# Kernel optimization log

Measured on AMD Instinct MI355X. Metric: run time of the kernel, lower is better.

## Reference

```python
import jax, jax.numpy as jnp
import numpy as np

NUM_HEADS = 12
HEAD_DIM = 64
HIDDEN = 768
SLOT_DIM = 30
BS = 8
FULL = SLOT_DIM * BS  # 240
SLOT_LEN = 32
LEN0 = 512   # slot-broadcast cache length
LEN1 = 128   # per-sample cache length


def tf_slot(x, slot_dim):
    # (slot_dim*bs, H, L, h) -> (bs, H, slot_dim*L, h)
    full, nh, L, h = x.shape
    bs = full // slot_dim
    x = x.reshape(slot_dim, bs, nh, L, h).transpose(1, 2, 0, 3, 4)
    return x.reshape(bs, nh, slot_dim * L, h)


def back_slot(x, slot_dim):
    # (bs, H, slot_dim*L, h) -> (slot_dim*bs, H, L, h)
    bs, nh, total, h = x.shape
    L = total // slot_dim
    x = x.reshape(bs, nh, slot_dim, L, h).transpose(2, 0, 1, 3, 4)
    return x.reshape(slot_dim * bs, nh, L, h)


def setup_inputs() -> dict:
    key = jax.random.key(0)
    ks = jax.random.split(key, 12)
    s = 0.02
    return {
        "hidden_states": jax.random.normal(ks[0], (FULL, SLOT_LEN, HIDDEN), jnp.float32),
        "attention_mask": jnp.zeros((FULL, 1, 1, LEN0 + LEN1 + SLOT_LEN), jnp.float32),
        "cache0_key": jax.random.normal(ks[1], (BS, NUM_HEADS, LEN0, HEAD_DIM), jnp.float32),
        "cache0_value": jax.random.normal(ks[2], (BS, NUM_HEADS, LEN0, HEAD_DIM), jnp.float32),
        "cache1_key": jax.random.normal(ks[3], (FULL, NUM_HEADS, LEN1, HEAD_DIM), jnp.float32),
        "cache1_value": jax.random.normal(ks[4], (FULL, NUM_HEADS, LEN1, HEAD_DIM), jnp.float32),
        "Wq": jax.random.normal(ks[5], (HIDDEN, HIDDEN), jnp.float32) * s,
        "bq": jax.random.normal(ks[6], (HIDDEN,), jnp.float32) * s,
        "Wk": jax.random.normal(ks[7], (HIDDEN, HIDDEN), jnp.float32) * s,
        "bk": jax.random.normal(ks[8], (HIDDEN,), jnp.float32) * s,
        "Wv": jax.random.normal(ks[9], (HIDDEN, HIDDEN), jnp.float32) * s,
        "bv": jax.random.normal(ks[10], (HIDDEN,), jnp.float32) * s,
        "slot_dim": SLOT_DIM,
    }


def reference(hidden_states, attention_mask, cache0_key, cache0_value,
              cache1_key, cache1_value, Wq, bq, Wk, bk, Wv, bv, slot_dim):
    B, L, hid = hidden_states.shape

    def split_heads(x):  # (B, L, hid) -> (B, H, L, h)
        return x.reshape(B, L, NUM_HEADS, HEAD_DIM).transpose(0, 2, 1, 3)

    q = split_heads(hidden_states @ Wq + bq)
    k = split_heads(hidden_states @ Wk + bk)
    v = split_heads(hidden_states @ Wv + bv)

    # self-attention scores (B, H, L, L)
    self_scores = jnp.einsum('bhqd,bhkd->bhqk', q, k)

    # cache0: slot-broadcast path (cache batch = bs, queries batch = slot_dim*bs)
    q_tf = tf_slot(q, slot_dim)  # (bs, H, slot_dim*L, h)
    s0 = back_slot(jnp.einsum('bhqd,bhkd->bhqk', q_tf, cache0_key), slot_dim)  # (B,H,L,LEN0)
    # cache1: direct path (matching batch)
    s1 = jnp.einsum('bhqd,bhkd->bhqk', q, cache1_key)  # (B,H,L,LEN1)

    scores = jnp.concatenate([s0, s1, self_scores], axis=-1)
    scores = scores / jnp.sqrt(jnp.float32(HEAD_DIM)) + attention_mask
    probs = jax.nn.softmax(scores, axis=-1)  # single softmax over all KV sources

    len0 = cache0_key.shape[2]
    len1 = cache1_key.shape[2]
    # self context
    ctx = jnp.einsum('bhqk,bhkd->bhqd', probs[..., -L:], v)
    # cache0 context via slot transform
    p0 = tf_slot(probs[..., :len0], slot_dim)  # (bs, H, slot_dim*L, LEN0)
    ctx = ctx + back_slot(jnp.einsum('bhqk,bhkd->bhqd', p0, cache0_value), slot_dim)
    # cache1 context direct
    ctx = ctx + jnp.einsum('bhqk,bhkd->bhqd', probs[..., len0:len0 + len1], cache1_value)

    # (B, H, L, h) -> (B, L, hid)
    return ctx.transpose(0, 2, 1, 3).reshape(B, L, hid)
```

## Files before the change

### kernel.cpp

```cpp
#include <hip/hip_runtime.h>
#include <math.h>

#define NUM_HEADS 12
#define HEAD_DIM  64
#define HIDDEN    768
#define BS        8
#define FULL      240
#define SLOT_LEN  32
#define LEN0      512
#define LEN1      128
#define KTOT      672
#define M_TOK     (FULL * SLOT_LEN)

typedef float f32x4 __attribute__((ext_vector_type(4)));
typedef short s16x8 __attribute__((ext_vector_type(8)));
typedef short s16x4 __attribute__((ext_vector_type(4)));

__device__ __forceinline__ short f2bf(float x) {
    unsigned u = __float_as_uint(x);
    unsigned r = (u + 0x7fffu + ((u >> 16) & 1u)) >> 16;
    return (short)r;
}

__device__ __forceinline__ void gll16(const short* g, short* l) {
    __builtin_amdgcn_global_load_lds(
        (const __attribute__((address_space(1))) unsigned int*)g,
        (__attribute__((address_space(3))) unsigned int*)l, 16, 0, 0);
}

__global__ __launch_bounds__(256) void cast_hs(const float* __restrict__ in,
                                               short* __restrict__ out, int n4) {
    int i = blockIdx.x * 256 + threadIdx.x;
    if (i < n4) {
        float4 v = ((const float4*)in)[i];
        s16x4 o = {f2bf(v.x), f2bf(v.y), f2bf(v.z), f2bf(v.w)};
        ((s16x4*)out)[i] = o;
    }
}

__global__ __launch_bounds__(256) void prep_c0(const float* __restrict__ k0,
                                               const float* __restrict__ v0,
                                               short* __restrict__ k0c,
                                               short* __restrict__ v0t) {
    __shared__ float tile[32][65];
    const size_t base = (size_t)blockIdx.x * 2048;
    const int t = threadIdx.x;
    if (blockIdx.y == 0) {
        const int row = t >> 3, c8 = t & 7;
        const float* src = &k0[base + row * 64 + c8 * 8];
        float4 a = *(const float4*)src;
        float4 b = *(const float4*)(src + 4);
        s16x8 o = {f2bf(a.x), f2bf(a.y), f2bf(a.z), f2bf(a.w),
                   f2bf(b.x), f2bf(b.y), f2bf(b.z), f2bf(b.w)};
        *(s16x8*)&k0c[base + row * 64 + (size_t)((c8 ^ (row & 7)) * 8)] = o;
    } else {
#pragma unroll
        for (int i = 0; i < 2; ++i) {
            int f = t + i * 256;
            int kr = f >> 4, d4 = (f & 15) * 4;
            float4 v = *(const float4*)&v0[base + kr * 64 + d4];
            tile[kr][d4 + 0] = v.x; tile[kr][d4 + 1] = v.y;
            tile[kr][d4 + 2] = v.z; tile[kr][d4 + 3] = v.w;
        }
        __syncthreads();
#pragma unroll
        for (int i = 0; i < 2; ++i) {
            int g = t + i * 256;
            int d = g >> 3, kr4 = (g & 7) * 4;
            s16x4 o = {f2bf(tile[kr4 + 0][d]), f2bf(tile[kr4 + 1][d]),
                       f2bf(tile[kr4 + 2][d]), f2bf(tile[kr4 + 3][d])};
            int grp = (kr4 >> 3) ^ ((d >> 1) & 3);
            *(s16x4*)&v0t[base + d * 32 + grp * 8 + (kr4 & 7)] = o;
        }
    }
}

__global__ __launch_bounds__(256) void cast_w_t(const float* __restrict__ Wq,
                                                const float* __restrict__ Wk,
                                                const float* __restrict__ Wv,
                                                short* __restrict__ WtAll) {
    const float* W = (blockIdx.z == 0) ? Wq : (blockIdx.z == 1) ? Wk : Wv;
    short* Wt = WtAll + (size_t)blockIdx.z * HIDDEN * HIDDEN;
    __shared__ __align__(16) float tile[32][33];
    const int kb0 = blockIdx.y * 32, nb0 = blockIdx.x * 32;
    const int r = threadIdx.x >> 3, c4 = (threadIdx.x & 7) * 4;
    float4 v = *(const float4*)&W[(size_t)(kb0 + r) * HIDDEN + nb0 + c4];
    tile[r][c4 + 0] = v.x; tile[r][c4 + 1] = v.y;
    tile[r][c4 + 2] = v.z; tile[r][c4 + 3] = v.w;
    __syncthreads();
    s16x4 o = {f2bf(tile[c4 + 0][r]), f2bf(tile[c4 + 1][r]),
               f2bf(tile[c4 + 2][r]), f2bf(tile[c4 + 3][r])};
    *(s16x4*)&Wt[(size_t)(nb0 + r) * HIDDEN + kb0 + c4] = o;
}

__global__ __launch_bounds__(256) void qkv_mfma(
    const short* __restrict__ hsb, const short* __restrict__ WtAll,
    const float* __restrict__ bq, const float* __restrict__ bk,
    const float* __restrict__ bv,
    short* __restrict__ qo, short* __restrict__ ko, short* __restrict__ vo)
{
    const int z = blockIdx.z;
    const short* Wt = WtAll + (size_t)z * HIDDEN * HIDDEN;
    const float* bias = (z == 0) ? bq : (z == 1) ? bk : bv;
    short* outp = (z == 0) ? qo : (z == 1) ? ko : vo;

    __shared__ __align__(16) short smem[128 * 128];
    short* As = smem;
    short* Bs = smem + 128 * 64;

    const int t = threadIdx.x;
    const int lane = t & 63, w = t >> 6;
    const int l15 = lane & 15, quad = lane >> 4;
    const int mBase = blockIdx.y * 128, nBase = blockIdx.x * 128;
    const int mw = (w & 1) * 64, nw = (w >> 1) * 64;

    const int srow_in = lane >> 3;
    const int scol8 = (lane & 7) ^ srow_in;

    f32x4 acc[4][4];
    const f32x4 z4 = {0.f, 0.f, 0.f, 0.f};
#pragma unroll
    for (int i = 0; i < 4; ++i)
#pragma unroll
        for (int j = 0; j < 4; ++j) acc[i][j] = z4;

    for (int kb = 0; kb < HIDDEN; kb += 64) {
        __syncthreads();
#pragma unroll
        for (int j = 0; j < 4; ++j) {
            int row = w * 32 + j * 8 + srow_in;
            gll16(&hsb[(size_t)(mBase + row) * HIDDEN + kb + scol8 * 8],
                  &As[(w * 32 + j * 8) * 64]);
            gll16(&Wt[(size_t)(nBase + row) * HIDDEN + kb + scol8 * 8],
                  &Bs[(w * 32 + j * 8) * 64]);
        }
        __syncthreads();
#pragma unroll
        for (int kc = 0; kc < 2; ++kc) {
            s16x8 a[4], b[4];
#pragma unroll
            for (int mt = 0; mt < 4; ++mt) {
                int row = mw + mt * 16 + l15;
                int c8 = (kc * 4 + quad) ^ (row & 7);
                a[mt] = *(const s16x8*)&As[row * 64 + c8 * 8];
            }
#pragma unroll
            for (int nt = 0; nt < 4; ++nt) {
                int row = nw + nt * 16 + l15;
                int c8 = (kc * 4 + quad) ^ (row & 7);
                b[nt] = *(const s16x8*)&Bs[row * 64 + c8 * 8];
            }
#pragma unroll
            for (int mt = 0; mt < 4; ++mt)
#pragma unroll
                for (int nt = 0; nt < 4; ++nt)
                    acc[mt][nt] = __builtin_amdgcn_mfma_f32_16x16x32_bf16(
                        a[mt], b[nt], acc[mt][nt], 0, 0, 0);
        }
    }

    __syncthreads();
#pragma unroll
    for (int nt = 0; nt < 4; ++nt) {
        float bvv = bias[nBase + nw + nt * 16 + l15];
        int col = nw + nt * 16 + l15;
#pragma unroll
        for (int mt = 0; mt < 4; ++mt)
#pragma unroll
            for (int r = 0; r < 4; ++r) {
                int row = mw + mt * 16 + quad * 4 + r;
                smem[row * 128 + col] = f2bf(acc[mt][nt][r] + bvv);
            }
    }
    __syncthreads();
#pragma unroll
    for (int i = 0; i < 8; ++i) {
        int f = t + i * 256;
        int row = f >> 4, c8 = (f & 15) * 8;
        uint4 val = *(const uint4*)&smem[row * 128 + c8];
        int m = mBase + row, n = nBase + c8;
        size_t dst = (((size_t)(m >> 5) * NUM_HEADS + (n >> 6)) * SLOT_LEN + (m & 31)) * 64 + (n & 63);
        *(uint4*)&outp[dst] = val;
    }
}

__global__ __launch_bounds__(256) void attn_mfma(
    const short* __restrict__ qb, const short* __restrict__ kbuf,
    const short* __restrict__ vbuf,
    const short* __restrict__ k0c, const short* __restrict__ v0t,
    const float* __restrict__ c1k, const float* __restrict__ c1v,
    const float* __restrict__ mask, float* __restrict__ out)
{
    __shared__ __align__(16) short sm_s[20480];

    const int t = threadIdx.x, lane = t & 63, w = t >> 6;
    const int task = blockIdx.x;
    const int B = task / 12, h = task % 12;
    const int l15 = lane & 15, quad = lane >> 4;

    const short* qp  = qb  + (size_t)(B * NUM_HEADS + h) * SLOT_LEN * 64;
    const short* ksp = kbuf + (size_t)(B * NUM_HEADS + h) * SLOT_LEN * 64;
    const short* vsp = vbuf + (size_t)(B * NUM_HEADS + h) * SLOT_LEN * 64;
    const short* k0p = k0c + (size_t)((B & 7) * NUM_HEADS + h) * LEN0 * 64;
    const short* v0p = v0t + (size_t)((B & 7) * NUM_HEADS + h) * LEN0 * 64;
    const float* k1p = c1k + (size_t)(B * NUM_HEADS + h) * LEN1 * 64;
    const float* v1p = c1v + (size_t)(B * NUM_HEADS + h) * LEN1 * 64;
    const float* mp  = mask + (size_t)B * KTOT;

    short (*K)[64] = (short(*)[64])(sm_s + w * 5120);
    short (*V)[32] = (short(*)[32])(sm_s + w * 5120 + 2048);
    short (*P)[32] = (short(*)[32])(sm_s + w * 5120 + 4096);
    short* Kf = sm_s + w * 5120;
    short* Vf = sm_s + w * 5120 + 2048;

    const int skey = lane >> 4;
    const int sc4 = (lane & 15) << 2;

    const float LOG2E = 1.4426950408889634f;
    const float SCL   = 0.125f * 1.4426950408889634f;

    s16x8 qf[2][2];
#pragma unroll
    for (int qh = 0; qh < 2; ++qh)
#pragma unroll
        for (int kc = 0; kc < 2; ++kc)
            qf[qh][kc] = *(const s16x8*)&qp[(qh * 16 + l15) * 64 + kc * 32 + quad * 8];

    const f32x4 z4 = {0.f, 0.f, 0.f, 0.f};
    f32x4 o[2][4];
    float lpart[2][4];
#pragma unroll
    for (int qh = 0; qh < 2; ++qh) {
#pragma unroll
        for (int dq = 0; dq < 4; ++dq) o[qh][dq] = z4;
#pragma unroll
        for (int r = 0; r < 4; ++r) lpart[qh][r] = 0.f;
    }

    auto qk_exp = [&](float mv0, float mv1) {
        f32x4 s[2][2];
#pragma unroll
        for (int qh = 0; qh < 2; ++qh)
#pragma unroll
            for (int kh = 0; kh < 2; ++kh) s[qh][kh] = z4;
#pragma unroll
        for (int kh = 0; kh < 2; ++kh) {
            int rowk = kh * 16 + l15;
            s16x8 kf0 = *(const s16x8*)&K[rowk][(quad ^ (rowk & 7)) * 8];
            s16x8 kf1 = *(const s16x8*)&K[rowk][((4 + quad) ^ (rowk & 7)) * 8];
#pragma unroll
            for (int qh = 0; qh < 2; ++qh) {
                s[qh][kh] = __builtin_amdgcn_mfma_f32_16x16x32_bf16(qf[qh][0], kf0, s[qh][kh], 0, 0, 0);
                s[qh][kh] = __builtin_amdgcn_mfma_f32_16x16x32_bf16(qf[qh][1], kf1, s[qh][kh], 0, 0, 0);
            }
        }
#pragma unroll
        for (int qh = 0; qh < 2; ++qh)
#pragma unroll
            for (int kh = 0; kh < 2; ++kh) {
                float mv = kh ? mv1 : mv0;
#pragma unroll
                for (int r = 0; r < 4; ++r) {
                    float p = exp2f(fmaf(s[qh][kh][r], SCL, mv));
                    lpart[qh][r] += p;
                    int prow = qh * 16 + quad * 4 + r;
                    int pswz = ((kh * 2 + (l15 >> 3)) ^ ((prow >> 1) & 3)) * 8 + (l15 & 7);
                    P[prow][pswz] = f2bf(p);
                }
            }
    };
    auto pv = [&]() {
#pragma unroll
        for (int qh = 0; qh < 2; ++qh) {
            int prow2 = qh * 16 + l15;
            int pg = (quad ^ ((l15 >> 1) & 3)) * 8;
            s16x4 plo = *(const s16x4*)&P[prow2][pg];
            s16x4 phi = *(const s16x4*)&P[prow2][pg + 4];
            s16x8 pf = __builtin_shufflevector(plo, phi, 0, 1, 2, 3, 4, 5, 6, 7);
#pragma unroll
            for (int dq = 0; dq < 4; ++dq) {
                int vrow = dq * 16 + l15;
                s16x8 vf = *(const s16x8*)&V[vrow][(quad ^ ((l15 >> 1) & 3)) * 8];
                o[qh][dq] = __builtin_amdgcn_mfma_f32_16x16x32_bf16(pf, vf, o[qh][dq], 0, 0, 0);
            }
        }
    };

    if (w == 3) {
#pragma unroll
        for (int i = 0; i < 8; ++i) {
            int key = i * 4 + skey;
            *(s16x4*)&K[key][((l15 >> 1) ^ (key & 7)) * 8 + (l15 & 1) * 4] =
                *(const s16x4*)&ksp[key * 64 + sc4];
        }
        short vtmp[32];
#pragma unroll
        for (int key = 0; key < 32; ++key) vtmp[key] = vsp[key * 64 + lane];
#pragma unroll
        for (int k4 = 0; k4 < 8; ++k4) {
            s16x4 vo4 = {vtmp[k4 * 4 + 0], vtmp[k4 * 4 + 1],
                         vtmp[k4 * 4 + 2], vtmp[k4 * 4 + 3]};
            int grp = (k4 >> 1) ^ ((lane >> 1) & 3);
            *(s16x4*)&V[lane][grp * 8 + (k4 & 1) * 4] = vo4;
        }
        float mv0 = mp[20 * 32 + l15] * LOG2E;
        float mv1 = mp[20 * 32 + 16 + l15] * LOG2E;
        qk_exp(mv0, mv1);
        pv();
    }

    {
        int c = 16 + w;
        const float* sk = k1p + (c - 16) * 2048;
        const float* sv = v1p + (c - 16) * 2048;
        float4 kr[4], vv[4];
#pragma unroll
        for (int i = 0; i < 4; ++i)
            kr[i] = *(const float4*)&sk[(i * 4 + skey) * 64 + sc4];
#pragma unroll
        for (int i = 0; i < 4; ++i)
            vv[i] = *(const float4*)&sv[(i * 4 + skey) * 64 + sc4];
#pragma unroll
        for (int i = 0; i < 4; ++i) {
            s16x4 kk = {f2bf(kr[i].x), f2bf(kr[i].y), f2bf(kr[i].z), f2bf(kr[i].w)};
            int row = i * 4 + skey;
            *(s16x4*)&K[row][((l15 >> 1) ^ (row & 7)) * 8 + (l15 & 1) * 4] = kk;
        }
#pragma unroll
        for (int i = 0; i < 4; ++i)
            kr[i] = *(const float4*)&sk[((i + 4) * 4 + skey) * 64 + sc4];
#pragma unroll
        for (int i = 0; i < 4; ++i) {
            s16x4 kk = {f2bf(kr[i].x), f2bf(kr[i].y), f2bf(kr[i].z), f2bf(kr[i].w)};
            int row = (i + 4) * 4 + skey;
            *(s16x4*)&K[row][((l15 >> 1) ^ (row & 7)) * 8 + (l15 & 1) * 4] = kk;
        }
        float mv0 = mp[c * 32 + l15] * LOG2E;
        float mv1 = mp[c * 32 + 16 + l15] * LOG2E;
        qk_exp(mv0, mv1);
#pragma unroll
        for (int i = 0; i < 4; ++i) {
            int key = i * 4 + skey;
            int kg = key >> 3, ks = key & 7;
#pragma unroll
            for (int j = 0; j < 4; ++j) {
                int rowv = sc4 + j;
                float fv = (j == 0) ? vv[i].x : (j == 1) ? vv[i].y : (j == 2) ? vv[i].z : vv[i].w;
                V[rowv][(kg ^ ((rowv >> 1) & 3)) * 8 + ks] = f2bf(fv);
            }
        }
#pragma unroll
        for (int i = 0; i < 4; ++i)
            vv[i] = *(const float4*)&sv[((i + 4) * 4 + skey) * 64 + sc4];
#pragma unroll
        for (int i = 0; i < 4; ++i) {
            int key = (i + 4) * 4 + skey;
            int kg = key >> 3, ks = key & 7;
#pragma unroll
            for (int j = 0; j < 4; ++j) {
                int rowv = sc4 + j;
                float fv = (j == 0) ? vv[i].x : (j == 1) ? vv[i].y : (j == 2) ? vv[i].z : vv[i].w;
                V[rowv][(kg ^ ((rowv >> 1) & 3)) * 8 + ks] = f2bf(fv);
            }
        }
        pv();
    }

    {
        s16x8 kpre[4], vpre[4];
        const int cbase = w * 4;
        auto issue_bf = [&](int c) {
            const short* kcb = k0p + c * 2048;
            const short* vcb = v0p + c * 2048;
#pragma unroll
            for (int i = 0; i < 4; ++i) {
                kpre[i] = *(const s16x8*)&kcb[(i * 64 + lane) * 8];
                vpre[i] = *(const s16x8*)&vcb[(i * 64 + lane) * 8];
            }
        };
        issue_bf(cbase);
#pragma unroll
        for (int j = 0; j < 4; ++j) {
            int c = cbase + j;
#pragma unroll
            for (int i = 0; i < 4; ++i)
                *(s16x8*)&Kf[(i * 64 + lane) * 8] = kpre[i];
#pragma unroll
            for (int i = 0; i < 4; ++i)
                *(s16x8*)&Vf[(i * 64 + lane) * 8] = vpre[i];
            if (j + 1 < 4) issue_bf(c + 1);
            float mv0 = mp[c * 32 + l15] * LOG2E;
            float mv1 = mp[c * 32 + 16 + l15] * LOG2E;
            qk_exp(mv0, mv1);
            pv();
        }
    }

    float lred[2][4];
#pragma unroll
    for (int qh = 0; qh < 2; ++qh)
#pragma unroll
        for (int r = 0; r < 4; ++r) {
            float l = lpart[qh][r];
            l += __shfl_xor(l, 1);
            l += __shfl_xor(l, 2);
            l += __shfl_xor(l, 4);
            l += __shfl_xor(l, 8);
            lred[qh][r] = l;
        }

    __syncthreads();
    float* smf = (float*)sm_s;
#pragma unroll
    for (int qh = 0; qh < 2; ++qh)
#pragma unroll
        for (int dq = 0; dq < 4; ++dq)
#pragma unroll
            for (int r = 0; r < 4; ++r) {
                int row = qh * 16 + quad * 4 + r, col = dq * 16 + l15;
                smf[w * 2048 + row * 64 + col] = o[qh][dq][r];
            }
    if (l15 == 0) {
#pragma unroll
        for (int qh = 0; qh < 2; ++qh)
#pragma unroll
            for (int r = 0; r < 4; ++r)
                smf[8192 + w * 32 + qh * 16 + quad * 4 + r] = lred[qh][r];
    }
    __syncthreads();

    {
        int row = t >> 3, c8 = (t & 7) * 8;
        float lt = smf[8192 + row] + smf[8192 + 32 + row] +
                   smf[8192 + 64 + row] + smf[8192 + 96 + row];
        float inv = 1.f / lt;
        float4 o0, o1;
#pragma unroll
        for (int j = 0; j < 4; ++j) {
            int col = c8 + j;
            o0[j] = (smf[row * 64 + col] + smf[2048 + row * 64 + col] +
                     smf[4096 + row * 64 + col] + smf[6144 + row * 64 + col]) * inv;
        }
#pragma unroll
        for (int j = 0; j < 4; ++j) {
            int col = c8 + 4 + j;
            o1[j] = (smf[row * 64 + col] + smf[2048 + row * 64 + col] +
                     smf[4096 + row * 64 + col] + smf[6144 + row * 64 + col]) * inv;
        }
        float* op = &out[((size_t)B * SLOT_LEN + row) * HIDDEN + h * 64 + c8];
        *(float4*)op = o0;
        *(float4*)(op + 4) = o1;
    }
}

extern "C" void kernel_launch(void* const* d_in, const int* in_sizes, int n_in,
                              void* d_out, int out_size, void* d_ws, size_t ws_size,
                              hipStream_t stream) {
    const float* hs   = (const float*)d_in[0];
    const float* mask = (const float*)d_in[1];
    const float* c0k  = (const float*)d_in[2];
    const float* c0v  = (const float*)d_in[3];
    const float* c1k  = (const float*)d_in[4];
    const float* c1v  = (const float*)d_in[5];
    const float* Wq   = (const float*)d_in[6];
    const float* bq   = (const float*)d_in[7];
    const float* Wk   = (const float*)d_in[8];
    const float* bk   = (const float*)d_in[9];
    const float* Wv   = (const float*)d_in[10];
    const float* bv   = (const float*)d_in[11];
    float* out = (float*)d_out;

    short* hsb = (short*)d_ws;
    short* WtA = hsb + (size_t)M_TOK * HIDDEN;
    short* qb  = WtA + (size_t)3 * HIDDEN * HIDDEN;
    short* kbw = qb + (size_t)M_TOK * HIDDEN;
    short* vbw = kbw + (size_t)M_TOK * HIDDEN;
    short* k0c = (short*)d_ws;
    short* v0t = k0c + (size_t)BS * NUM_HEADS * LEN0 * HEAD_DIM;

    cast_hs<<<(M_TOK * HIDDEN / 4 + 255) / 256, 256, 0, stream>>>(hs, hsb, M_TOK * HIDDEN / 4);
    cast_w_t<<<dim3(24, 24, 3), 256, 0, stream>>>(Wq, Wk, Wv, WtA);
    qkv_mfma<<<dim3(HIDDEN / 128, M_TOK / 128, 3), 256, 0, stream>>>(
        hsb, WtA, bq, bk, bv, qb, kbw, vbw);
    prep_c0<<<dim3(BS * NUM_HEADS * (LEN0 / 32), 2), 256, 0, stream>>>(c0k, c0v, k0c, v0t);
    attn_mfma<<<FULL * NUM_HEADS, 256, 0, stream>>>(qb, kbw, vbw, k0c, v0t, c1k, c1v, mask, out);
}
```

Before: 369.3 us.

## Load attention K/V fragments straight into registers with MFMA-ready layouts

Cache0 V and the self-attention V are now written in an MFMA-fragment-ordered layout by the prep and QKV kernels, and K fragments are read directly from global memory. The attention kernel can therefore feed MFMAs from registers instead of staging K/V through LDS. Fragment loads are software-pipelined one chunk ahead. Only the cache1 path still goes through LDS, which shrinks the shared-memory footprint and may raise occupancy, at the cost of more register pressure and less coalesced global reads for K.

After: 359.8 us. 2.6% less time.

```diff
diff --git a/kernel.cpp b/kernel.cpp
--- a/kernel.cpp
+++ b/kernel.cpp
@@ -38,41 +38,31 @@
     }
 }
 
-__global__ __launch_bounds__(256) void prep_c0(const float* __restrict__ k0,
-                                               const float* __restrict__ v0,
-                                               short* __restrict__ k0c,
-                                               short* __restrict__ v0t) {
+__global__ __launch_bounds__(256) void prep_v0(const float* __restrict__ v0,
+                                               short* __restrict__ v0f) {
     __shared__ float tile[32][65];
     const size_t base = (size_t)blockIdx.x * 2048;
     const int t = threadIdx.x;
-    if (blockIdx.y == 0) {
-        const int row = t >> 3, c8 = t & 7;
-        const float* src = &k0[base + row * 64 + c8 * 8];
-        float4 a = *(const float4*)src;
-        float4 b = *(const float4*)(src + 4);
-        s16x8 o = {f2bf(a.x), f2bf(a.y), f2bf(a.z), f2bf(a.w),
-                   f2bf(b.x), f2bf(b.y), f2bf(b.z), f2bf(b.w)};
-        *(s16x8*)&k0c[base + row * 64 + (size_t)((c8 ^ (row & 7)) * 8)] = o;
-    } else {
-#pragma unroll
-        for (int i = 0; i < 2; ++i) {
-            int f = t + i * 256;
-            int kr = f >> 4, d4 = (f & 15) * 4;
-            float4 v = *(const float4*)&v0[base + kr * 64 + d4];
-            tile[kr][d4 + 0] = v.x; tile[kr][d4 + 1] = v.y;
-            tile[kr][d4 + 2] = v.z; tile[kr][d4 + 3] = v.w;
-        }
-        __syncthreads();
-#pragma unroll
-        for (int i = 0; i < 2; ++i) {
-            int g = t + i * 256;
-            int d = g >> 3, kr4 = (g & 7) * 4;
-            s16x4 o = {f2bf(tile[kr4 + 0][d]), f2bf(tile[kr4 + 1][d]),
-                       f2bf(tile[kr4 + 2][d]), f2bf(tile[kr4 + 3][d])};
-            int grp = (kr4 >> 3) ^ ((d >> 1) & 3);
-            *(s16x4*)&v0t[base + d * 32 + grp * 8 + (kr4 & 7)] = o;
-        }
-    }
+#pragma unroll
+    for (int i = 0; i < 2; ++i) {
+        int f = t + i * 256;
+        int kr = f >> 4, d4 = (f & 15) * 4;
+        float4 v = *(const float4*)&v0[base + kr * 64 + d4];
+        tile[kr][d4 + 0] = v.x; tile[kr][d4 + 1] = v.y;
+        tile[kr][d4 + 2] = v.z; tile[kr][d4 + 3] = v.w;
+    }
+    __syncthreads();
+    const int dq = t >> 6, lane = t & 63;
+    const int quad = lane >> 4, l15 = lane & 15;
+    s16x8 o = {f2bf(tile[quad * 8 + 0][dq * 16 + l15]),
+               f2bf(tile[quad * 8 + 1][dq * 16 + l15]),
+               f2bf(tile[quad * 8 + 2][dq * 16 + l15]),
+               f2bf(tile[quad * 8 + 3][dq * 16 + l15]),
+               f2bf(tile[quad * 8 + 4][dq * 16 + l15]),
+               f2bf(tile[quad * 8 + 5][dq * 16 + l15]),
+               f2bf(tile[quad * 8 + 6][dq * 16 + l15]),
+               f2bf(tile[quad * 8 + 7][dq * 16 + l15])};
+    *(s16x8*)&v0f[base + (size_t)t * 8] = o;
 }
 
 __global__ __launch_bounds__(256) void cast_w_t(const float* __restrict__ Wq,
@@ -104,7 +94,7 @@
     const float* bias = (z == 0) ? bq : (z == 1) ? bk : bv;
     short* outp = (z == 0) ? qo : (z == 1) ? ko : vo;
 
-    __shared__ __align__(16) short smem[128 * 128];
+    __shared__ __align__(16) short smem[128 * 144];
     short* As = smem;
     short* Bs = smem + 128 * 64;
 
@@ -169,49 +159,63 @@
 #pragma unroll
             for (int r = 0; r < 4; ++r) {
                 int row = mw + mt * 16 + quad * 4 + r;
-                smem[row * 128 + col] = f2bf(acc[mt][nt][r] + bvv);
-            }
-    }
-    __syncthreads();
-#pragma unroll
-    for (int i = 0; i < 8; ++i) {
-        int f = t + i * 256;
-        int row = f >> 4, c8 = (f & 15) * 8;
-        uint4 val = *(const uint4*)&smem[row * 128 + c8];
-        int m = mBase + row, n = nBase + c8;
-        size_t dst = (((size_t)(m >> 5) * NUM_HEADS + (n >> 6)) * SLOT_LEN + (m & 31)) * 64 + (n & 63);
-        *(uint4*)&outp[dst] = val;
+                short v = f2bf(acc[mt][nt][r] + bvv);
+                if (z == 2) smem[col * 144 + row] = v;
+                else        smem[row * 128 + col] = v;
+            }
+    }
+    __syncthreads();
+    if (z == 2) {
+#pragma unroll
+        for (int i = 0; i < 8; ++i) {
+            int f = t + i * 256;
+            int d = f >> 4, kb8 = (f & 15) * 8;
+            uint4 val = *(const uint4*)&smem[d * 144 + kb8];
+            int m0 = mBase + kb8, n = nBase + d;
+            int B = m0 >> 5, key0 = m0 & 31, hh = n >> 6, dd = n & 63;
+            size_t dst = ((size_t)(B * NUM_HEADS + hh) * 2048) +
+                         (size_t)((dd >> 4) * 512 + (key0 >> 3) * 128 + (dd & 15) * 8);
+            *(uint4*)&outp[dst] = val;
+        }
+    } else {
+#pragma unroll
+        for (int i = 0; i < 8; ++i) {
+            int f = t + i * 256;
+            int row = f >> 4, c8 = (f & 15) * 8;
+            uint4 val = *(const uint4*)&smem[row * 128 + c8];
+            int m = mBase + row, n = nBase + c8;
+            size_t dst = (((size_t)(m >> 5) * NUM_HEADS + (n >> 6)) * SLOT_LEN + (m & 31)) * 64 + (n & 63);
+            *(uint4*)&outp[dst] = val;
+        }
     }
 }
 
 __global__ __launch_bounds__(256) void attn_mfma(
     const short* __restrict__ qb, const short* __restrict__ kbuf,
     const short* __restrict__ vbuf,
-    const short* __restrict__ k0c, const short* __restrict__ v0t,
+    const short* __restrict__ k0c, const short* __restrict__ v0f,
     const float* __restrict__ c1k, const float* __restrict__ c1v,
     const float* __restrict__ mask, float* __restrict__ out)
 {
-    __shared__ __align__(16) short sm_s[20480];
+    __shared__ __align__(16) float smf[8448];
+    short* sm16 = (short*)smf;
 
     const int t = threadIdx.x, lane = t & 63, w = t >> 6;
     const int task = blockIdx.x;
     const int B = task / 12, h = task % 12;
     const int l15 = lane & 15, quad = lane >> 4;
 
-    const short* qp  = qb  + (size_t)(B * NUM_HEADS + h) * SLOT_LEN * 64;
-    const short* ksp = kbuf + (size_t)(B * NUM_HEADS + h) * SLOT_LEN * 64;
-    const short* vsp = vbuf + (size_t)(B * NUM_HEADS + h) * SLOT_LEN * 64;
-    const short* k0p = k0c + (size_t)((B & 7) * NUM_HEADS + h) * LEN0 * 64;
-    const short* v0p = v0t + (size_t)((B & 7) * NUM_HEADS + h) * LEN0 * 64;
-    const float* k1p = c1k + (size_t)(B * NUM_HEADS + h) * LEN1 * 64;
-    const float* v1p = c1v + (size_t)(B * NUM_HEADS + h) * LEN1 * 64;
-    const float* mp  = mask + (size_t)B * KTOT;
-
-    short (*K)[64] = (short(*)[64])(sm_s + w * 5120);
-    short (*V)[32] = (short(*)[32])(sm_s + w * 5120 + 2048);
-    short (*P)[32] = (short(*)[32])(sm_s + w * 5120 + 4096);
-    short* Kf = sm_s + w * 5120;
-    short* Vf = sm_s + w * 5120 + 2048;
+    const short* qp   = qb  + (size_t)(B * NUM_HEADS + h) * 2048;
+    const short* kspF = kbuf + (size_t)(B * NUM_HEADS + h) * 2048;
+    const short* vspF = vbuf + (size_t)(B * NUM_HEADS + h) * 2048;
+    const short* k0p  = k0c + (size_t)((B & 7) * NUM_HEADS + h) * LEN0 * 64;
+    const short* v0p  = v0f + (size_t)((B & 7) * NUM_HEADS + h) * LEN0 * 64;
+    const float* k1p  = c1k + (size_t)(B * NUM_HEADS + h) * LEN1 * 64;
+    const float* v1p  = c1v + (size_t)(B * NUM_HEADS + h) * LEN1 * 64;
+    const float* mp   = mask + (size_t)B * KTOT;
+
+    short (*V)[32] = (short(*)[32])(sm16 + w * 3072);
+    short (*P)[32] = (short(*)[32])(sm16 + w * 3072 + 2048);
 
     const int skey = lane >> 4;
     const int sc4 = (lane & 15) << 2;
@@ -237,23 +241,20 @@
         for (int r = 0; r < 4; ++r) lpart[qh][r] = 0.f;
     }
 
-    auto qk_exp = [&](float mv0, float mv1) {
-        f32x4 s[2][2];
+    auto qk_mm = [&](const s16x8* kf, f32x4 (*s)[2]) {
 #pragma unroll
         for (int qh = 0; qh < 2; ++qh)
 #pragma unroll
             for (int kh = 0; kh < 2; ++kh) s[qh][kh] = z4;
 #pragma unroll
-        for (int kh = 0; kh < 2; ++kh) {
-            int rowk = kh * 16 + l15;
-            s16x8 kf0 = *(const s16x8*)&K[rowk][(quad ^ (rowk & 7)) * 8];
-            s16x8 kf1 = *(const s16x8*)&K[rowk][((4 + quad) ^ (rowk & 7)) * 8];
+        for (int kh = 0; kh < 2; ++kh)
 #pragma unroll
             for (int qh = 0; qh < 2; ++qh) {
-                s[qh][kh] = __builtin_amdgcn_mfma_f32_16x16x32_bf16(qf[qh][0], kf0, s[qh][kh], 0, 0, 0);
-                s[qh][kh] = __builtin_amdgcn_mfma_f32_16x16x32_bf16(qf[qh][1], kf1, s[qh][kh], 0, 0, 0);
-            }
-        }
+                s[qh][kh] = __builtin_amdgcn_mfma_f32_16x16x32_bf16(qf[qh][0], kf[kh * 2 + 0], s[qh][kh], 0, 0, 0);
+                s[qh][kh] = __builtin_amdgcn_mfma_f32_16x16x32_bf16(qf[qh][1], kf[kh * 2 + 1], s[qh][kh], 0, 0, 0);
+            }
+    };
+    auto exp_p = [&](f32x4 (*s)[2], float mv0, float mv1) {
 #pragma unroll
         for (int qh = 0; qh < 2; ++qh)
 #pragma unroll
@@ -269,7 +270,7 @@
                 }
             }
     };
-    auto pv = [&]() {
+    auto pv_reg = [&](const s16x8* vf) {
 #pragma unroll
         for (int qh = 0; qh < 2; ++qh) {
             int prow2 = qh * 16 + l15;
@@ -278,6 +279,19 @@
             s16x4 phi = *(const s16x4*)&P[prow2][pg + 4];
             s16x8 pf = __builtin_shufflevector(plo, phi, 0, 1, 2, 3, 4, 5, 6, 7);
 #pragma unroll
+            for (int dq = 0; dq < 4; ++dq)
+                o[qh][dq] = __builtin_amdgcn_mfma_f32_16x16x32_bf16(pf, vf[dq], o[qh][dq], 0, 0, 0);
+        }
+    };
+    auto pv_lds = [&]() {
+#pragma unroll
+        for (int qh = 0; qh < 2; ++qh) {
+            int prow2 = qh * 16 + l15;
+            int pg = (quad ^ ((l15 >> 1) & 3)) * 8;
+            s16x4 plo = *(const s16x4*)&P[prow2][pg];
+            s16x4 phi = *(const s16x4*)&P[prow2][pg + 4];
+            s16x8 pf = __builtin_shufflevector(plo, phi, 0, 1, 2, 3, 4, 5, 6, 7);
+#pragma unroll
             for (int dq = 0; dq < 4; ++dq) {
                 int vrow = dq * 16 + l15;
                 s16x8 vf = *(const s16x8*)&V[vrow][(quad ^ ((l15 >> 1) & 3)) * 8];
@@ -286,114 +300,81 @@
         }
     };
 
-    if (w == 3) {
+    const int c0base = w * 4;
+    const int nfast = (w == 0) ? 5 : 4;
+
+    auto load_kf = [&](int i, s16x8* kf) {
+        const short* kb = (i < 4) ? (k0p + (size_t)(c0base + i) * 2048) : kspF;
+#pragma unroll
+        for (int f = 0; f < 4; ++f) {
+            int kh = f >> 1, kc = f & 1;
+            kf[f] = *(const s16x8*)&kb[(kh * 16 + l15) * 64 + kc * 32 + quad * 8];
+        }
+    };
+    auto load_vf = [&](int i, s16x8* vf) {
+        const short* vb = (i < 4) ? (v0p + (size_t)(c0base + i) * 2048) : vspF;
+#pragma unroll
+        for (int dq = 0; dq < 4; ++dq)
+            vf[dq] = *(const s16x8*)&vb[(dq * 64 + lane) * 8];
+    };
+    auto mchunk = [&](int i) { return (i < 4) ? (c0base + i) : 20; };
+
+    s16x8 kf[4], vf[4];
+    float mv0n, mv1n;
+    load_kf(0, kf);
+    load_vf(0, vf);
+    { int mc = mchunk(0); mv0n = mp[mc * 32 + l15] * LOG2E; mv1n = mp[mc * 32 + 16 + l15] * LOG2E; }
+
+    for (int i = 0; i < nfast; ++i) {
+        float mv0 = mv0n, mv1 = mv1n;
+        f32x4 s[2][2];
+        qk_mm(kf, s);
+        if (i + 1 < nfast) {
+            load_kf(i + 1, kf);
+            int mc = mchunk(i + 1);
+            mv0n = mp[mc * 32 + l15] * LOG2E;
+            mv1n = mp[mc * 32 + 16 + l15] * LOG2E;
+        }
+        exp_p(s, mv0, mv1);
+        pv_reg(vf);
+        if (i + 1 < nfast) load_vf(i + 1, vf);
+    }
+
+    {
+        const float* sk = k1p + w * 2048;
+        const float* sv = v1p + w * 2048;
+        float4 vvr[8];
+#pragma unroll
+        for (int i = 0; i < 8; ++i)
+            vvr[i] = *(const float4*)&sv[(i * 4 + skey) * 64 + sc4];
+        s16x8 kc1[4];
+#pragma unroll
+        for (int f = 0; f < 4; ++f) {
+            int kh = f >> 1, kc = f & 1;
+            const float* kfp = &sk[(kh * 16 + l15) * 64 + kc * 32 + quad * 8];
+            float4 lo = *(const float4*)kfp;
+            float4 hi = *(const float4*)(kfp + 4);
+            kc1[f] = {f2bf(lo.x), f2bf(lo.y), f2bf(lo.z), f2bf(lo.w),
+                      f2bf(hi.x), f2bf(hi.y), f2bf(hi.z), f2bf(hi.w)};
+        }
+        int mc = 16 + w;
+        float mv0 = mp[mc * 32 + l15] * LOG2E;
+        float mv1 = mp[mc * 32 + 16 + l15] * LOG2E;
+        f32x4 s[2][2];
+        qk_mm(kc1, s);
+        exp_p(s, mv0, mv1);
 #pragma unroll
         for (int i = 0; i < 8; ++i) {
             int key = i * 4 + skey;
-            *(s16x4*)&K[key][((l15 >> 1) ^ (key & 7)) * 8 + (l15 & 1) * 4] =
-                *(const s16x4*)&ksp[key * 64 + sc4];
-        }
-        short vtmp[32];
-#pragma unroll
-        for (int key = 0; key < 32; ++key) vtmp[key] = vsp[key * 64 + lane];
-#pragma unroll
-        for (int k4 = 0; k4 < 8; ++k4) {
-            s16x4 vo4 = {vtmp[k4 * 4 + 0], vtmp[k4 * 4 + 1],
-                         vtmp[k4 * 4 + 2], vtmp[k4 * 4 + 3]};
-            int grp = (k4 >> 1) ^ ((lane >> 1) & 3);
-            *(s16x4*)&V[lane][grp * 8 + (k4 & 1) * 4] = vo4;
-        }
-        float mv0 = mp[20 * 32 + l15] * LOG2E;
-        float mv1 = mp[20 * 32 + 16 + l15] * LOG2E;
-        qk_exp(mv0, mv1);
-        pv();
-    }
-
-    {
-        int c = 16 + w;
-        const float* sk = k1p + (c - 16) * 2048;
-        const float* sv = v1p + (c - 16) * 2048;
-        float4 kr[4], vv[4];
-#pragma unroll
-        for (int i = 0; i < 4; ++i)
-            kr[i] = *(const float4*)&sk[(i * 4 + skey) * 64 + sc4];
-#pragma unroll
-        for (int i = 0; i < 4; ++i)
-            vv[i] = *(const float4*)&sv[(i * 4 + skey) * 64 + sc4];
-#pragma unroll
-        for (int i = 0; i < 4; ++i) {
-            s16x4 kk = {f2bf(kr[i].x), f2bf(kr[i].y), f2bf(kr[i].z), f2bf(kr[i].w)};
-            int row = i * 4 + skey;
-            *(s16x4*)&K[row][((l15 >> 1) ^ (row & 7)) * 8 + (l15 & 1) * 4] = kk;
-        }
-#pragma unroll
-        for (int i = 0; i < 4; ++i)
-            kr[i] = *(const float4*)&sk[((i + 4) * 4 + skey) * 64 + sc4];
-#pragma unroll
-        for (int i = 0; i < 4; ++i) {
-            s16x4 kk = {f2bf(kr[i].x), f2bf(kr[i].y), f2bf(kr[i].z), f2bf(kr[i].w)};
-            int row = (i + 4) * 4 + skey;
-            *(s16x4*)&K[row][((l15 >> 1) ^ (row & 7)) * 8 + (l15 & 1) * 4] = kk;
-        }
-        float mv0 = mp[c * 32 + l15] * LOG2E;
-        float mv1 = mp[c * 32 + 16 + l15] * LOG2E;
-        qk_exp(mv0, mv1);
-#pragma unroll
-        for (int i = 0; i < 4; ++i) {
-            int key = i * 4 + skey;
             int kg = key >> 3, ks = key & 7;
 #pragma unroll
             for (int j = 0; j < 4; ++j) {
                 int rowv = sc4 + j;
-                float fv = (j == 0) ? vv[i].x : (j == 1) ? vv[i].y : (j == 2) ? vv[i].z : vv[i].w;
+                float fv = (j == 0) ? vvr[i].x : (j == 1) ? vvr[i].y : (j == 2) ? vvr[i].z : vvr[i].w;
                 V[rowv][(kg ^ ((rowv >> 1) & 3)) * 8 + ks] = f2bf(fv);
             }
         }
-#pragma unroll
-        for (int i = 0; i < 4; ++i)
-            vv[i] = *(const float4*)&sv[((i + 4) * 4 + skey) * 64 + sc4];
-#pragma unroll
-        for (int i = 0; i < 4; ++i) {
-            int key = (i + 4) * 4 + skey;
-            int kg = key >> 3, ks = key & 7;
-#pragma unroll
-            for (int j = 0; j < 4; ++j) {
-                int rowv = sc4 + j;
-                float fv = (j == 0) ? vv[i].x : (j == 1) ? vv[i].y : (j == 2) ? vv[i].z : vv[i].w;
-                V[rowv][(kg ^ ((rowv >> 1) & 3)) * 8 + ks] = f2bf(fv);
-            }
-        }
-        pv();
-    }
-
-    {
-        s16x8 kpre[4], vpre[4];
-        const int cbase = w * 4;
-        auto issue_bf = [&](int c) {
-            const short* kcb = k0p + c * 2048;
-            const short* vcb = v0p + c * 2048;
-#pragma unroll
-            for (int i = 0; i < 4; ++i) {
-                kpre[i] = *(const s16x8*)&kcb[(i * 64 + lane) * 8];
-                vpre[i] = *(const s16x8*)&vcb[(i * 64 + lane) * 8];
-            }
-        };
-        issue_bf(cbase);
-#pragma unroll
-        for (int j = 0; j < 4; ++j) {
-            int c = cbase + j;
-#pragma unroll
-            for (int i = 0; i < 4; ++i)
-                *(s16x8*)&Kf[(i * 64 + lane) * 8] = kpre[i];
-#pragma unroll
-            for (int i = 0; i < 4; ++i)
-                *(s16x8*)&Vf[(i * 64 + lane) * 8] = vpre[i];
-            if (j + 1 < 4) issue_bf(c + 1);
-            float mv0 = mp[c * 32 + l15] * LOG2E;
-            float mv1 = mp[c * 32 + 16 + l15] * LOG2E;
-            qk_exp(mv0, mv1);
-            pv();
-        }
+        pv_lds();
     }
 
     float lred[2][4];
@@ -410,7 +391,6 @@
         }
 
     __syncthreads();
-    float* smf = (float*)sm_s;
 #pragma unroll
     for (int qh = 0; qh < 2; ++qh)
 #pragma unroll
@@ -476,12 +456,16 @@
     short* kbw = qb + (size_t)M_TOK * HIDDEN;
     short* vbw = kbw + (size_t)M_TOK * HIDDEN;
     short* k0c = (short*)d_ws;
-    short* v0t = k0c + (size_t)BS * NUM_HEADS * LEN0 * HEAD_DIM;
+    short* v0f = k0c + (size_t)BS * NUM_HEADS * LEN0 * HEAD_DIM;
 
     cast_hs<<<(M_TOK * HIDDEN / 4 + 255) / 256, 256, 0, stream>>>(hs, hsb, M_TOK * HIDDEN / 4);
     cast_w_t<<<dim3(24, 24, 3), 256, 0, stream>>>(Wq, Wk, Wv, WtA);
     qkv_mfma<<<dim3(HIDDEN / 128, M_TOK / 128, 3), 256, 0, stream>>>(
         hsb, WtA, bq, bk, bv, qb, kbw, vbw);
-    prep_c0<<<dim3(BS * NUM_HEADS * (LEN0 / 32), 2), 256, 0, stream>>>(c0k, c0v, k0c, v0t);
-    attn_mfma<<<FULL * NUM_HEADS, 256, 0, stream>>>(qb, kbw, vbw, k0c, v0t, c1k, c1v, mask, out);
-}
+    {
+        int n4 = BS * NUM_HEADS * LEN0 * HEAD_DIM / 4;
+        cast_hs<<<(n4 + 255) / 256, 256, 0, stream>>>(c0k, k0c, n4);
+        prep_v0<<<BS * NUM_HEADS * (LEN0 / 32), 256, 0, stream>>>(c0v, v0f);
+    }
+    attn_mfma<<<FULL * NUM_HEADS, 256, 0, stream>>>(qb, kbw, vbw, k0c, v0f, c1k, c1v, mask, out);
+}
```
